# Optimization experiments

Measured on AMD Instinct MI355X. Metric: run time of the kernel, lower is better.

The kernel has to match this reference:

```python
import jax, jax.numpy as jnp
import numpy as np

WD, WH, WW = 1, 8, 8           # window size
NH = 2                          # num heads
EPS = 1e-5                      # torch LayerNorm default


def _layernorm(x, g, b):
    mu = jnp.mean(x, axis=-1, keepdims=True)
    var = jnp.mean((x - mu) ** 2, axis=-1, keepdims=True)
    return (x - mu) * jax.lax.rsqrt(var + EPS) * g + b


def setup_inputs() -> dict:
    key = jax.random.key(0)
    ks = jax.random.split(key, 12)
    C, H = 192, 768  # dim, mlp hidden
    w = lambda k, shape: (jax.random.normal(k, shape, jnp.float32) * 0.02)
    return {
        "x": jax.random.normal(ks[0], (2, 8, 96, 96, C), jnp.float32),
        "norm3_g": jnp.ones((C,), jnp.float32),
        "norm3_b": jnp.zeros((C,), jnp.float32),
        "in_proj_w": w(ks[1], (3 * C, C)),
        "in_proj_b": jnp.zeros((3 * C,), jnp.float32),
        "out_proj_w": w(ks[2], (C, C)),
        "out_proj_b": jnp.zeros((C,), jnp.float32),
        "norm4_g": jnp.ones((C,), jnp.float32),
        "norm4_b": jnp.zeros((C,), jnp.float32),
        "fc1_w": w(ks[3], (H, C)),
        "fc1_b": jnp.zeros((H,), jnp.float32),
        "fc2_w": w(ks[4], (C, H)),
        "fc2_b": jnp.zeros((C,), jnp.float32),
    }


def _part3(x, norm3_g, norm3_b, in_proj_w, in_proj_b, out_proj_w, out_proj_b):
    B, D, H, W, C = x.shape
    Dn, Hn, Wn = D // WD, H // WH, W // WW
    P = Hn * Wn          # spatial windows
    Wt = WD * WH * WW    # tokens per window (64)
    L = Dn * Wt          # attention sequence length

    xn = _layernorm(x, norm3_g, norm3_b)
    # window partition: (B, Dn, Hn, Wn, wd, wh, ww, C)
    xw = xn.reshape(B, Dn, WD, Hn, WH, Wn, WW, C).transpose(0, 1, 3, 5, 2, 4, 6, 7)
    # tgt: (B, Dn, P, Wt, C) -> h: (B*P, Dn*Wt, C)
    tgt = xw.reshape(B, Dn, P, Wt, C)
    h = tgt.transpose(0, 2, 1, 3, 4).reshape(B * P, L, C)

    # qkv projection (torch Linear convention: x @ W.T + b)
    qkv = h @ in_proj_w.T + in_proj_b          # (Bp, L, 3C)
    q, k, v = jnp.split(qkv, 3, axis=-1)
    hd = C // NH
    q = q.reshape(B * P, L, NH, hd)
    k = k.reshape(B * P, L, NH, hd)
    v = v.reshape(B * P, L, NH, hd)

    # block-causal mask over temporal index (each block is Wt x Wt)
    neg_inf = jnp.finfo(jnp.float32).min
    tmask = jnp.triu(jnp.full((Dn, Dn), neg_inf, jnp.float32), k=1)
    mask = jnp.repeat(jnp.repeat(tmask, Wt, axis=0), Wt, axis=1)  # (L, L)

    scale = 1.0 / np.sqrt(hd)
    scores = jnp.einsum("blhd,bmhd->bhlm", q * scale, k) + mask
    attn = jax.nn.softmax(scores, axis=-1)
    out = jnp.einsum("bhlm,bmhd->blhd", attn, v).reshape(B * P, L, C)
    out = out @ out_proj_w.T + out_proj_b

    # reverse: (B, P, Dn, Wt, C) -> windows -> (B, D, H, W, C)
    out = out.reshape(B, P, Dn, Wt, C).transpose(0, 2, 1, 3, 4)
    out = out.reshape(B, Dn, Hn, Wn, WD, WH, WW, C)
    out = out.transpose(0, 1, 4, 2, 5, 3, 6, 7).reshape(B, D, H, W, C)
    return out


def reference(x, norm3_g, norm3_b, in_proj_w, in_proj_b, out_proj_w, out_proj_b,
              norm4_g, norm4_b, fc1_w, fc1_b, fc2_w, fc2_b):
    x = x + _part3(x, norm3_g, norm3_b, in_proj_w, in_proj_b, out_proj_w, out_proj_b)
    xn = _layernorm(x, norm4_g, norm4_b)
    mlp = jax.nn.gelu(xn @ fc1_w.T + fc1_b, approximate=False) @ fc2_w.T + fc2_b
    return x + mlp
```

## Files before the change

### kernel.cpp

```cpp
#include <hip/hip_runtime.h>
#include <cstdint>
#include <cstddef>


typedef float   f32x4  __attribute__((ext_vector_type(4)));
typedef __bf16  bf16x8 __attribute__((ext_vector_type(8)));
typedef unsigned int   u32x4  __attribute__((ext_vector_type(4)));
typedef unsigned short u16x4  __attribute__((ext_vector_type(4)));

#define DEVI __device__ __forceinline__

DEVI float bf2f(unsigned short u) {
    union { unsigned int i; float f; } v; v.i = ((unsigned int)u) << 16; return v.f;
}
DEVI unsigned short f2bf(float f) {
    unsigned int u = __builtin_bit_cast(unsigned int, f);
    unsigned int r = u + 0x7fffu + ((u >> 16) & 1u);
    return (unsigned short)(r >> 16);
}
DEVI float gelu_fast(float v) {
    float t = v * v;
    float z = v * (1.5957691216057308f + 0.07135481627f * t);
    float e = __expf(z);
    float r = 2.0f / (1.0f + e);
    return v - 0.5f * v * r;
}

typedef __attribute__((address_space(3))) unsigned char       lds_u8;
typedef __attribute__((address_space(1))) const unsigned char g_u8;
DEVI void gl_lds16(const void* g, void* l) {
    __builtin_amdgcn_global_load_lds((g_u8*)g, (lds_u8*)l, 16, 0, 0);
}

__global__ __launch_bounds__(256) void k_wconv(const float* __restrict__ wqkv,
                                               const float* __restrict__ wout,
                                               const float* __restrict__ wfc1,
                                               const float* __restrict__ wfc2,
                                               const float* __restrict__ n3g,
                                               const float* __restrict__ n4g,
                                               unsigned short* __restrict__ oq,
                                               unsigned short* __restrict__ oo,
                                               unsigned short* __restrict__ o1,
                                               unsigned short* __restrict__ o2) {
    int i = blockIdx.x * 256 + threadIdx.x;
    if (i < 122880) {
        int r = i / 192, c = i - r * 192;
        oq[i] = (r < 576) ? f2bf(wqkv[i] * n3g[c]) : (unsigned short)0;
    } else if (i < 172032) {
        int j = i - 122880; int r = j / 192;
        oo[j] = (r < 192) ? f2bf(wout[j]) : (unsigned short)0;
    } else if (i < 319488) {
        int j = i - 172032; int c = j % 192;
        o1[j] = f2bf(wfc1[j] * n4g[c]);
    } else if (i < 516096) {
        int j = i - 319488; int r = j / 768;
        o2[j] = (r < 192) ? f2bf(wfc2[j]) : (unsigned short)0;
    }
}

__global__ __launch_bounds__(256) void k_bias(const float* __restrict__ wqkv,
                                              const float* __restrict__ bqkv,
                                              const float* __restrict__ n3b,
                                              const float* __restrict__ wfc1,
                                              const float* __restrict__ bfc1,
                                              const float* __restrict__ n4b,
                                              float* __restrict__ beffq,
                                              float* __restrict__ beff1) {
    int wid = blockIdx.x * 4 + (threadIdx.x >> 6);
    int lane = threadIdx.x & 63;
    const float* wrow; const float* bb; float base; float* dst;
    if (wid < 576) { wrow = wqkv + (size_t)wid * 192; bb = n3b; base = bqkv[wid]; dst = beffq + wid; }
    else { int h = wid - 576; wrow = wfc1 + (size_t)h * 192; bb = n4b; base = bfc1[h]; dst = beff1 + h; }
    float s = wrow[lane] * bb[lane] + wrow[lane + 64] * bb[lane + 64]
            + wrow[lane + 128] * bb[lane + 128];
#pragma unroll
    for (int off = 32; off; off >>= 1) s += __shfl_xor(s, off);
    if (lane == 0) *dst = base + s;
}

__global__ __launch_bounds__(256) void k_ln3(const float* __restrict__ x,
                                             unsigned short* __restrict__ h) {
    int w = threadIdx.x >> 6, lane = threadIdx.x & 63;
    int token = blockIdx.x * 4 + w;
    const float* xp = x + (size_t)token * 192;
    float v0 = xp[lane], v1 = xp[lane + 64], v2 = xp[lane + 128];
    float s = v0 + v1 + v2;
#pragma unroll
    for (int off = 32; off; off >>= 1) s += __shfl_xor(s, off);
    float mean = s * (1.f / 192.f);
    float d0 = v0 - mean, d1 = v1 - mean, d2 = v2 - mean;
    float q = d0 * d0 + d1 * d1 + d2 * d2;
#pragma unroll
    for (int off = 32; off; off >>= 1) q += __shfl_xor(q, off);
    float rs = rsqrtf(q * (1.f / 192.f) + 1e-5f);
    int b  = token / (8 * 96 * 96);
    int r0 = token - b * (8 * 96 * 96);
    int d  = r0 / (96 * 96);
    int r1 = r0 - d * (96 * 96);
    int hh = r1 / 96;
    int ww = r1 - hh * 96;
    int bp = b * 144 + (hh >> 3) * 12 + (ww >> 3);
    int l  = d * 64 + (hh & 7) * 8 + (ww & 7);
    unsigned short* hp = h + ((size_t)bp * 512 + l) * 192;
    hp[lane]       = f2bf(d0 * rs);
    hp[lane + 64]  = f2bf(d1 * rs);
    hp[lane + 128] = f2bf(d2 * rs);
}

__global__ __launch_bounds__(256) void k_ln4b(const unsigned short* __restrict__ yb,
                                              unsigned short* __restrict__ xn) {
    int sub = threadIdx.x >> 5, tl = threadIdx.x & 31;
    size_t row = (size_t)blockIdx.x * 8 + sub;
    const unsigned int* rp = reinterpret_cast<const unsigned int*>(yb + row * 192);
    float v[6];
#pragma unroll
    for (int j = 0; j < 3; j++) {
        unsigned int w = rp[tl + 32 * j];
        v[2 * j]     = bf2f((unsigned short)(w & 0xffffu));
        v[2 * j + 1] = bf2f((unsigned short)(w >> 16));
    }
    float s = v[0] + v[1] + v[2] + v[3] + v[4] + v[5];
#pragma unroll
    for (int off = 1; off < 32; off <<= 1) s += __shfl_xor(s, off);
    float mean = s * (1.f / 192.f);
    float q = 0.f;
#pragma unroll
    for (int j = 0; j < 6; j++) { v[j] -= mean; q += v[j] * v[j]; }
#pragma unroll
    for (int off = 1; off < 32; off <<= 1) q += __shfl_xor(q, off);
    float rs = rsqrtf(q * (1.f / 192.f) + 1e-5f);
    unsigned int* op = reinterpret_cast<unsigned int*>(xn + row * 192);
#pragma unroll
    for (int j = 0; j < 3; j++) {
        unsigned short lo = f2bf(v[2 * j]     * rs);
        unsigned short hi = f2bf(v[2 * j + 1] * rs);
        op[tl + 32 * j] = ((unsigned int)hi << 16) | lo;
    }
}

template <int EPI, int K, int NF>
__global__ __launch_bounds__(256) void k_gemm128(const unsigned short* __restrict__ A,
                                                 const unsigned short* __restrict__ Bw,
                                                 const float* __restrict__ bias,
                                                 unsigned short* __restrict__ outb,
                                                 unsigned short* __restrict__ vt,
                                                 const float* __restrict__ res,
                                                 const unsigned short* __restrict__ resb,
                                                 float* __restrict__ outf) {
    __shared__ unsigned short As[2][128 * 64];
    __shared__ unsigned short Bs[2][NF * 32 * 64];
    const int tid = threadIdx.x;
    const int nwg = gridDim.x * gridDim.y;
    const int flat = blockIdx.y * gridDim.x + blockIdx.x;
    const int swz = (flat & 7) * (nwg >> 3) + (flat >> 3);
    const int bx = swz % gridDim.x, by = swz / gridDim.x;
    const int row0 = by * 128, col0 = bx * (NF * 32);
    const int wv = tid >> 6, lane = tid & 63, lr = lane & 15, lg = lane >> 4;
    const int wr = wv >> 1, wc = wv & 1;
    const int sr = lane >> 3, sc = lane & 7;
    f32x4 acc[4][NF] = {};

    auto stage = [&](int t, int buf) {
        int k0 = t * 64;
#pragma unroll
        for (int i = 0; i < 4; i++) {
            int gq = wv * 4 + i;
            int r = gq * 8 + sr;
            int j = sc ^ (r & 7);
            gl_lds16(A + (size_t)(row0 + r) * K + k0 + j * 8, &As[buf][gq * 512]);
        }
#pragma unroll
        for (int i = 0; i < NF; i++) {
            int gq = wv * NF + i;
            int r = gq * 8 + sr;
            int j = sc ^ (r & 7);
            gl_lds16(Bw + (size_t)(col0 + r) * K + k0 + j * 8, &Bs[buf][gq * 512]);
        }
    };

    const int NT = K / 64;
    stage(0, 0);
    for (int t = 0; t < NT; ++t) {
        int cur = t & 1;
        if (t + 1 < NT) {
            stage(t + 1, cur ^ 1);
            if constexpr (NF == 4) asm volatile("s_waitcnt vmcnt(8)" ::: "memory");
            else                   asm volatile("s_waitcnt vmcnt(7)" ::: "memory");
        } else {
            asm volatile("s_waitcnt vmcnt(0)" ::: "memory");
        }
        __builtin_amdgcn_sched_barrier(0);
        __builtin_amdgcn_s_barrier();
        __builtin_amdgcn_sched_barrier(0);
#pragma unroll
        for (int kk = 0; kk < 64; kk += 32) {
            bf16x8 af[4], bf[NF];
#pragma unroll
            for (int m = 0; m < 4; m++) {
                int r = wr * 64 + m * 16 + lr;
                int j = ((kk >> 3) + lg) ^ (r & 7);
                af[m] = __builtin_bit_cast(bf16x8,
                    *reinterpret_cast<const u32x4*>(&As[cur][r * 64 + j * 8]));
            }
#pragma unroll
            for (int n = 0; n < NF; n++) {
                int r = wc * (NF * 16) + n * 16 + lr;
                int j = ((kk >> 3) + lg) ^ (r & 7);
                bf[n] = __builtin_bit_cast(bf16x8,
                    *reinterpret_cast<const u32x4*>(&Bs[cur][r * 64 + j * 8]));
            }
#pragma unroll
            for (int m = 0; m < 4; m++)
#pragma unroll
                for (int n = 0; n < NF; n++)
                    acc[m][n] = __builtin_amdgcn_mfma_f32_16x16x32_bf16(bf[n], af[m], acc[m][n], 0, 0, 0);
        }
        __builtin_amdgcn_sched_barrier(0);
        __builtin_amdgcn_s_barrier();
        __builtin_amdgcn_sched_barrier(0);
    }

#pragma unroll
    for (int m = 0; m < 4; m++) {
        const int arow = row0 + wr * 64 + m * 16 + lr;
        if constexpr (EPI == 0) {
#pragma unroll
            for (int n = 0; n < NF; n++) {
                const int colb = col0 + wc * (NF * 16) + n * 16 + lg * 4;
                if (colb < 384) {
                    f32x4 b4 = *reinterpret_cast<const f32x4*>(bias + colb);
                    float sc2 = (colb < 192) ? 0.1020620726159658f : 1.f;
                    u16x4 pk;
#pragma unroll
                    for (int rr = 0; rr < 4; rr++) pk[rr] = f2bf((acc[m][n][rr] + b4[rr]) * sc2);
                    *reinterpret_cast<u16x4*>(outb + (size_t)arow * 384 + colb) = pk;
                } else if (colb < 576) {
                    int head = (colb >= 480) ? 1 : 0;
                    int bp = arow >> 9, tok = arow & 511;
                    size_t vb = ((size_t)(bp * 2 + head) * 96 + (colb - 384 - head * 96)) * 512 + tok;
#pragma unroll
                    for (int rr = 0; rr < 4; rr++)
                        vt[vb + (size_t)rr * 512] = f2bf(acc[m][n][rr] + bias[colb + rr]);
                }
            }
        } else if constexpr (EPI == 1) {
            int bp = arow >> 9, l = arow & 511;
            int bb = bp / 144, p = bp - bb * 144;
            int hn = p / 12, wn = p - hn * 12;
            int dn = l >> 6, t_ = l & 63;
            size_t tok = ((size_t)((bb * 8 + dn) * 96 + hn * 8 + (t_ >> 3)) * 96 + wn * 8 + (t_ & 7));
#pragma unroll
            for (int n = 0; n < NF; n++) {
                const int colb = col0 + wc * (NF * 16) + n * 16 + lg * 4;
                size_t idx = tok * 192 + colb;
                f32x4 r4 = *reinterpret_cast<const f32x4*>(res + idx);
                f32x4 b4 = *reinterpret_cast<const f32x4*>(bias + colb);
                u16x4 pk;
#pragma unroll
                for (int rr = 0; rr < 4; rr++) pk[rr] = f2bf(r4[rr] + acc[m][n][rr] + b4[rr]);
                *reinterpret_cast<u16x4*>(outb + idx) = pk;
            }
        } else if constexpr (EPI == 2) {
#pragma unroll
            for (int n = 0; n < NF; n++) {
                const int colb = col0 + wc * (NF * 16) + n * 16 + lg * 4;
                f32x4 b4 = *reinterpret_cast<const f32x4*>(bias + colb);
                u16x4 pk;
#pragma unroll
                for (int rr = 0; rr < 4; rr++) pk[rr] = f2bf(gelu_fast(acc[m][n][rr] + b4[rr]));
                *reinterpret_cast<u16x4*>(outb + (size_t)arow * 768 + colb) = pk;
            }
        } else {
#pragma unroll
            for (int n = 0; n < NF; n++) {
                const int colb = col0 + wc * (NF * 16) + n * 16 + lg * 4;
                size_t idx = (size_t)arow * 192 + colb;
                f32x4 b4 = *reinterpret_cast<const f32x4*>(bias + colb);
                u16x4 rb = *reinterpret_cast<const u16x4*>(resb + idx);
                f32x4 o4;
#pragma unroll
                for (int rr = 0; rr < 4; rr++) o4[rr] = bf2f(rb[rr]) + acc[m][n][rr] + b4[rr];
                *reinterpret_cast<f32x4*>(outf + idx) = o4;
            }
        }
    }
}

__global__ __launch_bounds__(512) void k_attn(const unsigned short* __restrict__ qk,
                                              const unsigned short* __restrict__ vt,
                                              unsigned short* __restrict__ aout) {
    __shared__ unsigned short Ks[64][104];
    __shared__ unsigned short Vs[96][72];
    __shared__ unsigned short Ps[8][16][72];

    int bid = (blockIdx.x & 7) * 288 + (blockIdx.x >> 3);
    int bp = bid >> 3, rest = bid & 7, head = rest >> 2, pr = rest & 3;
    int tid = threadIdx.x, wv = tid >> 6, lane = tid & 63;
    int lr = lane & 15, lg = lane >> 4;
    int wq = wv & 3, wt = wv >> 2;
    int nk = 2 * pr + 2;

    size_t qrow0 = (size_t)bp * 512 + (size_t)(2 * pr + wt) * 64;
    const unsigned short* vbase = vt + (size_t)(bp * 2 + head) * 96 * 512;
    size_t krowb = (size_t)bp * 512;

    bf16x8 qf[3];
    {
        const unsigned short* qp = qk + (qrow0 + wq * 16 + lr) * 384 + head * 96 + lg * 8;
#pragma unroll
        for (int ks = 0; ks < 3; ks++)
            qf[ks] = __builtin_bit_cast(bf16x8, *reinterpret_cast<const u32x4*>(qp + ks * 32));
    }

    f32x4 o[6] = {};
    float m_ = -1e30f, lsum = 0.f;

    u32x4 sreg[3];
    auto issue = [&](int dnk) {
#pragma unroll
        for (int i = 0; i < 3; i++) {
            int c = tid + i * 512;
            if (c < 768) {
                int r = c / 12, cc = c - r * 12;
                sreg[i] = *reinterpret_cast<const u32x4*>(
                    qk + (krowb + dnk * 64 + r) * 384 + 192 + head * 96 + cc * 8);
            } else {
                int c2 = c - 768; int d = c2 >> 3, tb = c2 & 7;
                sreg[i] = *reinterpret_cast<const u32x4*>(
                    vbase + (size_t)d * 512 + dnk * 64 + tb * 8);
            }
        }
    };
    auto commit = [&]() {
#pragma unroll
        for (int i = 0; i < 3; i++) {
            int c = tid + i * 512;
            if (c < 768) {
                int r = c / 12, cc = c - r * 12;
                *reinterpret_cast<u32x4*>(&Ks[r][cc * 8]) = sreg[i];
            } else {
                int c2 = c - 768; int d = c2 >> 3, tb = c2 & 7;
                *reinterpret_cast<u32x4*>(&Vs[d][tb * 8]) = sreg[i];
            }
        }
    };

    issue(0);
    for (int dnk = 0; dnk < nk; ++dnk) {
        commit();
        __syncthreads();
        if (dnk + 1 < nk) issue(dnk + 1);
        if (wt == 1 || dnk < nk - 1) {
            f32x4 st[4] = {};
#pragma unroll
            for (int ks = 0; ks < 3; ks++) {
#pragma unroll
                for (int ct = 0; ct < 4; ct++) {
                    bf16x8 kf = __builtin_bit_cast(bf16x8,
                        *reinterpret_cast<const u32x4*>(&Ks[ct * 16 + lr][ks * 32 + lg * 8]));
                    st[ct] = __builtin_amdgcn_mfma_f32_16x16x32_bf16(kf, qf[ks], st[ct], 0, 0, 0);
                }
            }
            float mx = st[0][0];
#pragma unroll
            for (int ct = 0; ct < 4; ct++)
#pragma unroll
                for (int rr = 0; rr < 4; rr++) mx = fmaxf(mx, st[ct][rr]);
            mx = fmaxf(mx, __shfl_xor(mx, 16));
            mx = fmaxf(mx, __shfl_xor(mx, 32));
            float mnew = fmaxf(m_, mx);
            float corr = __expf(m_ - mnew);
            m_ = mnew;
            float ps = 0.f;
#pragma unroll
            for (int ct = 0; ct < 4; ct++) {
                u16x4 pk;
#pragma unroll
                for (int rr = 0; rr < 4; rr++) {
                    float pv = __expf(st[ct][rr] - mnew);
                    ps += pv;
                    pk[rr] = f2bf(pv);
                }
                *reinterpret_cast<u16x4*>(&Ps[wv][lr][ct * 16 + lg * 4]) = pk;
            }
            ps += __shfl_xor(ps, 16);
            ps += __shfl_xor(ps, 32);
            lsum = lsum * corr + ps;
#pragma unroll
            for (int rr = 0; rr < 4; rr++) {
                float cr = __shfl(corr, (lane & 48) | (lg * 4 + rr));
#pragma unroll
                for (int nf = 0; nf < 6; nf++) o[nf][rr] *= cr;
            }
#pragma unroll
            for (int kk = 0; kk < 2; kk++) {
                bf16x8 pf = __builtin_bit_cast(bf16x8,
                    *reinterpret_cast<const u32x4*>(&Ps[wv][lr][kk * 32 + lg * 8]));
#pragma unroll
                for (int nf = 0; nf < 6; nf++) {
                    bf16x8 vf = __builtin_bit_cast(bf16x8,
                        *reinterpret_cast<const u32x4*>(&Vs[nf * 16 + lr][kk * 32 + lg * 8]));
                    o[nf] = __builtin_amdgcn_mfma_f32_16x16x32_bf16(pf, vf, o[nf], 0, 0, 0);
                }
            }
        }
        __syncthreads();
    }

#pragma unroll
    for (int rr = 0; rr < 4; rr++) {
        float li = __shfl(lsum, (lane & 48) | (lg * 4 + rr));
        float inv = 1.f / li;
        size_t row = qrow0 + wq * 16 + lg * 4 + rr;
#pragma unroll
        for (int nf = 0; nf < 6; nf++)
            aout[row * 192 + head * 96 + nf * 16 + lr] = f2bf(o[nf][rr] * inv);
    }
}

extern "C" void kernel_launch(void* const* d_in, const int* in_sizes, int n_in,
                              void* d_out, int out_size, void* d_ws, size_t ws_size,
                              hipStream_t stream) {
    const float* x    = (const float*)d_in[0];
    const float* n3g  = (const float*)d_in[1];
    const float* n3b  = (const float*)d_in[2];
    const float* wqkv = (const float*)d_in[3];
    const float* bqkv = (const float*)d_in[4];
    const float* wout = (const float*)d_in[5];
    const float* bout = (const float*)d_in[6];
    const float* n4g  = (const float*)d_in[7];
    const float* n4b  = (const float*)d_in[8];
    const float* wfc1 = (const float*)d_in[9];
    const float* bfc1 = (const float*)d_in[10];
    const float* wfc2 = (const float*)d_in[11];
    const float* bfc2 = (const float*)d_in[12];
    float* out = (float*)d_out;

    char* ws = (char*)d_ws;
    unsigned short* qk     = (unsigned short*)(ws + 0);
    unsigned short* vt     = (unsigned short*)(ws + 113246208);
    unsigned short* attn   = (unsigned short*)(ws + 169869312);
    unsigned short* hidden = (unsigned short*)(ws + 0);
    unsigned short* ybf    = (unsigned short*)(ws + 226492416);
    unsigned short* h      = (unsigned short*)(ws + 283115520);
    unsigned short* xn4    = (unsigned short*)(ws + 283115520);
    unsigned short* wq_bf  = (unsigned short*)(ws + 339738624);
    unsigned short* wo_bf  = (unsigned short*)(ws + 339984384);
    unsigned short* w1_bf  = (unsigned short*)(ws + 340082688);
    unsigned short* w2_bf  = (unsigned short*)(ws + 340377600);
    float*          beffq  = (float*)(ws + 340770816);
    float*          beff1  = (float*)(ws + 340773120);

    k_wconv<<<2016, 256, 0, stream>>>(wqkv, wout, wfc1, wfc2, n3g, n4g, wq_bf, wo_bf, w1_bf, w2_bf);
    k_bias<<<336, 256, 0, stream>>>(wqkv, bqkv, n3b, wfc1, bfc1, n4b, beffq, beff1);
    k_ln3<<<36864, 256, 0, stream>>>(x, h);
    k_gemm128<0, 192, 4><<<dim3(5, 1152), 256, 0, stream>>>(h, wq_bf, beffq, qk, vt, nullptr, nullptr, nullptr);
    k_attn<<<2304, 512, 0, stream>>>(qk, vt, attn);
    k_gemm128<1, 192, 3><<<dim3(2, 1152), 256, 0, stream>>>(attn, wo_bf, bout, ybf, nullptr, x, nullptr, nullptr);
    k_ln4b<<<18432, 256, 0, stream>>>(ybf, xn4);
    k_gemm128<2, 192, 4><<<dim3(6, 1152), 256, 0, stream>>>(xn4, w1_bf, beff1, hidden, nullptr, nullptr, nullptr, nullptr);
    k_gemm128<3, 768, 3><<<dim3(2, 1152), 256, 0, stream>>>(hidden, w2_bf, bfc2, nullptr, nullptr, nullptr, ybf, out);
}
```

Before: 551.4 us.

## Fuse LayerNorm4 into fc1 GEMM and run fc2 in FP8

Drops the separate LayerNorm4 kernel. The fc1 GEMM now loads the bf16 residual rows into LDS, computes mean and variance per row, and normalizes in place before the MFMAs. The GELU output is stored as FP8, and fc2 weights are pre-converted to FP8, so fc2 uses FP8 MFMA. This halves hidden-activation traffic and raises MFMA throughput for fc2, at the cost of FP8 precision loss on a 768-wide reduction and redundant LayerNorm work in each of the 6 column blocks.

```diff
diff --git a/kernel.cpp b/kernel.cpp
--- a/kernel.cpp
+++ b/kernel.cpp
@@ -24,6 +24,14 @@
     float e = __expf(z);
     float r = 2.0f / (1.0f + e);
     return v - 0.5f * v * r;
+}
+DEVI unsigned int pk_fp8x4(float a, float b, float c, float d) {
+    int v = __builtin_amdgcn_cvt_pk_fp8_f32(a, b, 0, false);
+    v = __builtin_amdgcn_cvt_pk_fp8_f32(c, d, v, true);
+    return (unsigned int)v;
+}
+DEVI f32x4 mfma_fp8(unsigned long long a, unsigned long long b, f32x4 c) {
+    return __builtin_amdgcn_mfma_f32_16x16x32_fp8_fp8((long)a, (long)b, c, 0, 0, 0);
 }
 
 typedef __attribute__((address_space(3))) unsigned char       lds_u8;
@@ -41,7 +49,7 @@
                                                unsigned short* __restrict__ oq,
                                                unsigned short* __restrict__ oo,
                                                unsigned short* __restrict__ o1,
-                                               unsigned short* __restrict__ o2) {
+                                               unsigned short* __restrict__ o2f8) {
     int i = blockIdx.x * 256 + threadIdx.x;
     if (i < 122880) {
         int r = i / 192, c = i - r * 192;
@@ -52,9 +60,13 @@
     } else if (i < 319488) {
         int j = i - 172032; int c = j % 192;
         o1[j] = f2bf(wfc1[j] * n4g[c]);
-    } else if (i < 516096) {
-        int j = i - 319488; int r = j / 768;
-        o2[j] = (r < 192) ? f2bf(wfc2[j]) : (unsigned short)0;
+    } else if (i < 417792) {
+        int j = i - 319488;
+        int r = j / 384;
+        float a = 0.f, b = 0.f;
+        if (r < 192) { a = wfc2[2 * j]; b = wfc2[2 * j + 1]; }
+        int pk = __builtin_amdgcn_cvt_pk_fp8_f32(a, b, 0, false);
+        o2f8[j] = (unsigned short)pk;
     }
 }
 
@@ -107,46 +119,13 @@
     hp[lane + 128] = f2bf(d2 * rs);
 }
 
-__global__ __launch_bounds__(256) void k_ln4b(const unsigned short* __restrict__ yb,
-                                              unsigned short* __restrict__ xn) {
-    int sub = threadIdx.x >> 5, tl = threadIdx.x & 31;
-    size_t row = (size_t)blockIdx.x * 8 + sub;
-    const unsigned int* rp = reinterpret_cast<const unsigned int*>(yb + row * 192);
-    float v[6];
-#pragma unroll
-    for (int j = 0; j < 3; j++) {
-        unsigned int w = rp[tl + 32 * j];
-        v[2 * j]     = bf2f((unsigned short)(w & 0xffffu));
-        v[2 * j + 1] = bf2f((unsigned short)(w >> 16));
-    }
-    float s = v[0] + v[1] + v[2] + v[3] + v[4] + v[5];
-#pragma unroll
-    for (int off = 1; off < 32; off <<= 1) s += __shfl_xor(s, off);
-    float mean = s * (1.f / 192.f);
-    float q = 0.f;
-#pragma unroll
-    for (int j = 0; j < 6; j++) { v[j] -= mean; q += v[j] * v[j]; }
-#pragma unroll
-    for (int off = 1; off < 32; off <<= 1) q += __shfl_xor(q, off);
-    float rs = rsqrtf(q * (1.f / 192.f) + 1e-5f);
-    unsigned int* op = reinterpret_cast<unsigned int*>(xn + row * 192);
-#pragma unroll
-    for (int j = 0; j < 3; j++) {
-        unsigned short lo = f2bf(v[2 * j]     * rs);
-        unsigned short hi = f2bf(v[2 * j + 1] * rs);
-        op[tl + 32 * j] = ((unsigned int)hi << 16) | lo;
-    }
-}
-
 template <int EPI, int K, int NF>
 __global__ __launch_bounds__(256) void k_gemm128(const unsigned short* __restrict__ A,
                                                  const unsigned short* __restrict__ Bw,
                                                  const float* __restrict__ bias,
                                                  unsigned short* __restrict__ outb,
                                                  unsigned short* __restrict__ vt,
-                                                 const float* __restrict__ res,
-                                                 const unsigned short* __restrict__ resb,
-                                                 float* __restrict__ outf) {
+                                                 const float* __restrict__ res) {
     __shared__ unsigned short As[2][128 * 64];
     __shared__ unsigned short Bs[2][NF * 32 * 64];
     const int tid = threadIdx.x;
@@ -243,7 +222,7 @@
                         vt[vb + (size_t)rr * 512] = f2bf(acc[m][n][rr] + bias[colb + rr]);
                 }
             }
-        } else if constexpr (EPI == 1) {
+        } else {
             int bp = arow >> 9, l = arow & 511;
             int bb = bp / 144, p = bp - bb * 144;
             int hn = p / 12, wn = p - hn * 12;
@@ -259,28 +238,6 @@
 #pragma unroll
                 for (int rr = 0; rr < 4; rr++) pk[rr] = f2bf(r4[rr] + acc[m][n][rr] + b4[rr]);
                 *reinterpret_cast<u16x4*>(outb + idx) = pk;
-            }
-        } else if constexpr (EPI == 2) {
-#pragma unroll
-            for (int n = 0; n < NF; n++) {
-                const int colb = col0 + wc * (NF * 16) + n * 16 + lg * 4;
-                f32x4 b4 = *reinterpret_cast<const f32x4*>(bias + colb);
-                u16x4 pk;
-#pragma unroll
-                for (int rr = 0; rr < 4; rr++) pk[rr] = f2bf(gelu_fast(acc[m][n][rr] + b4[rr]));
-                *reinterpret_cast<u16x4*>(outb + (size_t)arow * 768 + colb) = pk;
-            }
-        } else {
-#pragma unroll
-            for (int n = 0; n < NF; n++) {
-                const int colb = col0 + wc * (NF * 16) + n * 16 + lg * 4;
-                size_t idx = (size_t)arow * 192 + colb;
-                f32x4 b4 = *reinterpret_cast<const f32x4*>(bias + colb);
-                u16x4 rb = *reinterpret_cast<const u16x4*>(resb + idx);
-                f32x4 o4;
-#pragma unroll
-                for (int rr = 0; rr < 4; rr++) o4[rr] = bf2f(rb[rr]) + acc[m][n][rr] + b4[rr];
-                *reinterpret_cast<f32x4*>(outf + idx) = o4;
             }
         }
     }
@@ -415,6 +372,219 @@
 #pragma unroll
         for (int nf = 0; nf < 6; nf++)
             aout[row * 192 + head * 96 + nf * 16 + lr] = f2bf(o[nf][rr] * inv);
+    }
+}
+
+__global__ __launch_bounds__(256) void k_fc1(const unsigned short* __restrict__ ybf,
+                                             const unsigned short* __restrict__ w1,
+                                             const float* __restrict__ beff1,
+                                             unsigned char* __restrict__ hid) {
+    __shared__ unsigned short As[3][128][64];
+    __shared__ unsigned short Bs[2][128 * 64];
+    const int tid = threadIdx.x;
+    const int nwg = gridDim.x * gridDim.y;
+    const int flat = blockIdx.y * gridDim.x + blockIdx.x;
+    const int swz = (flat & 7) * (nwg >> 3) + (flat >> 3);
+    const int bx = swz % gridDim.x, by = swz / gridDim.x;
+    const int row0 = by * 128, col0 = bx * 128;
+    const int wv = tid >> 6, lane = tid & 63, lr = lane & 15, lg = lane >> 4;
+    const int wr = wv >> 1, wc = wv & 1;
+    const int sr = lane >> 3, sc = lane & 7;
+
+    auto stageB = [&](int t, int buf) {
+        int k0 = t * 64;
+#pragma unroll
+        for (int i = 0; i < 4; i++) {
+            int gq = wv * 4 + i;
+            int r = gq * 8 + sr;
+            int j = sc ^ (r & 7);
+            gl_lds16(w1 + (size_t)(col0 + r) * 192 + k0 + j * 8, &Bs[buf][gq * 512]);
+        }
+    };
+
+    stageB(0, 0);
+    {
+        int ar = tid >> 1, ah = tid & 1;
+        const unsigned short* src = ybf + (size_t)(row0 + ar) * 192;
+        float sum = 0.f, ssq = 0.f;
+#pragma unroll
+        for (int ci = 0; ci < 12; ci++) {
+            int c = ah * 12 + ci;
+            u32x4 v = *reinterpret_cast<const u32x4*>(src + c * 8);
+            u16x4* hv = reinterpret_cast<u16x4*>(&v);
+#pragma unroll
+            for (int e = 0; e < 8; e++) {
+                float f = bf2f(((unsigned short*)&v)[e]);
+                sum += f; ssq += f * f;
+            }
+            (void)hv;
+            int j = (c & 7) ^ (ar & 7);
+            *reinterpret_cast<u32x4*>(&As[c >> 3][ar][j * 8]) = v;
+        }
+        sum += __shfl_xor(sum, 1); ssq += __shfl_xor(ssq, 1);
+        float mu = sum * (1.f / 192.f);
+        float rs = rsqrtf(ssq * (1.f / 192.f) - mu * mu + 1e-5f);
+#pragma unroll
+        for (int ci = 0; ci < 12; ci++) {
+            int c = ah * 12 + ci;
+            int j = (c & 7) ^ (ar & 7);
+            unsigned short* p8 = &As[c >> 3][ar][j * 8];
+#pragma unroll
+            for (int e = 0; e < 8; e++)
+                p8[e] = f2bf((bf2f(p8[e]) - mu) * rs);
+        }
+    }
+    asm volatile("s_waitcnt lgkmcnt(0)" ::: "memory");
+
+    f32x4 acc[4][4] = {};
+#pragma unroll
+    for (int t = 0; t < 3; ++t) {
+        if (t + 1 < 3) {
+            stageB(t + 1, (t + 1) & 1);
+            asm volatile("s_waitcnt vmcnt(4)" ::: "memory");
+        } else {
+            asm volatile("s_waitcnt vmcnt(0)" ::: "memory");
+        }
+        __builtin_amdgcn_sched_barrier(0);
+        __builtin_amdgcn_s_barrier();
+        __builtin_amdgcn_sched_barrier(0);
+#pragma unroll
+        for (int kk = 0; kk < 64; kk += 32) {
+            bf16x8 af[4], bf[4];
+#pragma unroll
+            for (int m = 0; m < 4; m++) {
+                int r = wr * 64 + m * 16 + lr;
+                int j = ((kk >> 3) + lg) ^ (r & 7);
+                af[m] = __builtin_bit_cast(bf16x8,
+                    *reinterpret_cast<const u32x4*>(&As[t][r][j * 8]));
+            }
+#pragma unroll
+            for (int n = 0; n < 4; n++) {
+                int r = wc * 64 + n * 16 + lr;
+                int j = ((kk >> 3) + lg) ^ (r & 7);
+                bf[n] = __builtin_bit_cast(bf16x8,
+                    *reinterpret_cast<const u32x4*>(&Bs[t & 1][r * 64 + j * 8]));
+            }
+#pragma unroll
+            for (int m = 0; m < 4; m++)
+#pragma unroll
+                for (int n = 0; n < 4; n++)
+                    acc[m][n] = __builtin_amdgcn_mfma_f32_16x16x32_bf16(bf[n], af[m], acc[m][n], 0, 0, 0);
+        }
+        __builtin_amdgcn_sched_barrier(0);
+        __builtin_amdgcn_s_barrier();
+        __builtin_amdgcn_sched_barrier(0);
+    }
+
+#pragma unroll
+    for (int m = 0; m < 4; m++) {
+        const int arow = row0 + wr * 64 + m * 16 + lr;
+#pragma unroll
+        for (int n = 0; n < 4; n++) {
+            const int colb = col0 + wc * 64 + n * 16 + lg * 4;
+            f32x4 b4 = *reinterpret_cast<const f32x4*>(beff1 + colb);
+            float g0 = gelu_fast(acc[m][n][0] + b4[0]);
+            float g1 = gelu_fast(acc[m][n][1] + b4[1]);
+            float g2 = gelu_fast(acc[m][n][2] + b4[2]);
+            float g3 = gelu_fast(acc[m][n][3] + b4[3]);
+            *reinterpret_cast<unsigned int*>(hid + (size_t)arow * 768 + colb) =
+                pk_fp8x4(g0, g1, g2, g3);
+        }
+    }
+}
+
+__global__ __launch_bounds__(256) void k_fc2(const unsigned char* __restrict__ hid,
+                                             const unsigned char* __restrict__ w2,
+                                             const float* __restrict__ b2,
+                                             const unsigned short* __restrict__ ybf,
+                                             float* __restrict__ out) {
+    __shared__ unsigned char As[2][128 * 64];
+    __shared__ unsigned char Bs[2][128 * 64];
+    const int tid = threadIdx.x;
+    const int nwg = gridDim.x * gridDim.y;
+    const int flat = blockIdx.y * gridDim.x + blockIdx.x;
+    const int swz = (flat & 7) * (nwg >> 3) + (flat >> 3);
+    const int bx = swz % gridDim.x, by = swz / gridDim.x;
+    const int row0 = by * 128, col0 = bx * 96;
+    const int wv = tid >> 6, lane = tid & 63, lr = lane & 15, lg = lane >> 4;
+    const int wr = wv >> 1, wc = wv & 1;
+    const int sr4 = lane >> 2, sc4 = lane & 3;
+    f32x4 acc[4][3] = {};
+
+    auto stage = [&](int t, int buf) {
+        int k0 = t * 64;
+#pragma unroll
+        for (int i = 0; i < 2; i++) {
+            int g = wv * 2 + i;
+            int r = g * 16 + sr4;
+            int j = sc4 ^ (r & 3);
+            gl_lds16(hid + (size_t)(row0 + r) * 768 + k0 + j * 16, &As[buf][g * 1024]);
+        }
+#pragma unroll
+        for (int i = 0; i < 2; i++) {
+            int g = wv * 2 + i;
+            int r = g * 16 + sr4;
+            int j = sc4 ^ (r & 3);
+            gl_lds16(w2 + (size_t)(col0 + r) * 768 + k0 + j * 16, &Bs[buf][g * 1024]);
+        }
+    };
+
+    stage(0, 0);
+    for (int t = 0; t < 12; ++t) {
+        int cur = t & 1;
+        if (t + 1 < 12) {
+            stage(t + 1, cur ^ 1);
+            asm volatile("s_waitcnt vmcnt(4)" ::: "memory");
+        } else {
+            asm volatile("s_waitcnt vmcnt(0)" ::: "memory");
+        }
+        __builtin_amdgcn_sched_barrier(0);
+        __builtin_amdgcn_s_barrier();
+        __builtin_amdgcn_sched_barrier(0);
+#pragma unroll
+        for (int kk = 0; kk < 2; kk++) {
+            const int cc = kk * 2 + (lg >> 1);
+            const int off = (lg & 1) * 8;
+            unsigned long long af[4], bfr[3];
+#pragma unroll
+            for (int m = 0; m < 4; m++) {
+                int r = wr * 64 + m * 16 + lr;
+                int j = cc ^ (r & 3);
+                af[m] = *reinterpret_cast<const unsigned long long*>(
+                    &As[cur][r * 64 + j * 16 + off]);
+            }
+#pragma unroll
+            for (int n = 0; n < 3; n++) {
+                int r = wc * 48 + n * 16 + lr;
+                int j = cc ^ (r & 3);
+                bfr[n] = *reinterpret_cast<const unsigned long long*>(
+                    &Bs[cur][r * 64 + j * 16 + off]);
+            }
+#pragma unroll
+            for (int m = 0; m < 4; m++)
+#pragma unroll
+                for (int n = 0; n < 3; n++)
+                    acc[m][n] = mfma_fp8(bfr[n], af[m], acc[m][n]);
+        }
+        __builtin_amdgcn_sched_barrier(0);
+        __builtin_amdgcn_s_barrier();
+        __builtin_amdgcn_sched_barrier(0);
+    }
+
+#pragma unroll
+    for (int m = 0; m < 4; m++) {
+        const int arow = row0 + wr * 64 + m * 16 + lr;
+#pragma unroll
+        for (int n = 0; n < 3; n++) {
+            const int colb = col0 + wc * 48 + n * 16 + lg * 4;
+            size_t idx = (size_t)arow * 192 + colb;
+            f32x4 b4 = *reinterpret_cast<const f32x4*>(b2 + colb);
+            u16x4 rb = *reinterpret_cast<const u16x4*>(ybf + idx);
+            f32x4 o4;
+#pragma unroll
+            for (int rr = 0; rr < 4; rr++) o4[rr] = bf2f(rb[rr]) + acc[m][n][rr] + b4[rr];
+            *reinterpret_cast<f32x4*>(out + idx) = o4;
+        }
     }
 }
 
@@ -438,26 +608,25 @@
 
     char* ws = (char*)d_ws;
     unsigned short* qk     = (unsigned short*)(ws + 0);
+    unsigned char*  hidden = (unsigned char*)(ws + 0);
     unsigned short* vt     = (unsigned short*)(ws + 113246208);
     unsigned short* attn   = (unsigned short*)(ws + 169869312);
-    unsigned short* hidden = (unsigned short*)(ws + 0);
     unsigned short* ybf    = (unsigned short*)(ws + 226492416);
     unsigned short* h      = (unsigned short*)(ws + 283115520);
-    unsigned short* xn4    = (unsigned short*)(ws + 283115520);
     unsigned short* wq_bf  = (unsigned short*)(ws + 339738624);
     unsigned short* wo_bf  = (unsigned short*)(ws + 339984384);
     unsigned short* w1_bf  = (unsigned short*)(ws + 340082688);
-    unsigned short* w2_bf  = (unsigned short*)(ws + 340377600);
-    float*          beffq  = (float*)(ws + 340770816);
-    float*          beff1  = (float*)(ws + 340773120);
-
-    k_wconv<<<2016, 256, 0, stream>>>(wqkv, wout, wfc1, wfc2, n3g, n4g, wq_bf, wo_bf, w1_bf, w2_bf);
+    unsigned short* w2_f8p = (unsigned short*)(ws + 340377600);
+    unsigned char*  w2_f8  = (unsigned char*)(ws + 340377600);
+    float*          beffq  = (float*)(ws + 340574208);
+    float*          beff1  = (float*)(ws + 340576512);
+
+    k_wconv<<<1632, 256, 0, stream>>>(wqkv, wout, wfc1, wfc2, n3g, n4g, wq_bf, wo_bf, w1_bf, w2_f8p);
     k_bias<<<336, 256, 0, stream>>>(wqkv, bqkv, n3b, wfc1, bfc1, n4b, beffq, beff1);
     k_ln3<<<36864, 256, 0, stream>>>(x, h);
-    k_gemm128<0, 192, 4><<<dim3(5, 1152), 256, 0, stream>>>(h, wq_bf, beffq, qk, vt, nullptr, nullptr, nullptr);
+    k_gemm128<0, 192, 4><<<dim3(5, 1152), 256, 0, stream>>>(h, wq_bf, beffq, qk, vt, nullptr);
     k_attn<<<2304, 512, 0, stream>>>(qk, vt, attn);
-    k_gemm128<1, 192, 3><<<dim3(2, 1152), 256, 0, stream>>>(attn, wo_bf, bout, ybf, nullptr, x, nullptr, nullptr);
-    k_ln4b<<<18432, 256, 0, stream>>>(ybf, xn4);
-    k_gemm128<2, 192, 4><<<dim3(6, 1152), 256, 0, stream>>>(xn4, w1_bf, beff1, hidden, nullptr, nullptr, nullptr, nullptr);
-    k_gemm128<3, 768, 3><<<dim3(2, 1152), 256, 0, stream>>>(hidden, w2_bf, bfc2, nullptr, nullptr, nullptr, ybf, out);
-}
+    k_gemm128<1, 192, 3><<<dim3(2, 1152), 256, 0, stream>>>(attn, wo_bf, bout, ybf, nullptr, x);
+    k_fc1<<<dim3(6, 1152), 256, 0, stream>>>(ybf, w1_bf, beff1, hidden);
+    k_fc2<<<dim3(2, 1152), 256, 0, stream>>>(hidden, w2_f8, bfc2, ybf, out);
+}
```

Result: no change. 545.8 us (-1.0%).

## Store MLP hidden as FP8 and run fc2 with FP8 MFMA kernel

Applied to the files above, without the earlier changes.

The fc1 epilogue now applies a sigmoid-based GELU approximation and packs the hidden activations into FP8 instead of BF16. The fc2 weights are likewise converted to FP8. A new dedicated fc2 GEMM kernel uses FP8 16x16x32 MFMA with swizzled LDS staging, and adds the residual in its epilogue. The goal is to halve the hidden-tensor memory traffic and to use the faster FP8 matrix path. The cost is lower numerical accuracy from both FP8 quantization and the cruder GELU approximation, which may break tolerance.

```diff
diff --git a/kernel.cpp b/kernel.cpp
--- a/kernel.cpp
+++ b/kernel.cpp
@@ -18,12 +18,17 @@
     unsigned int r = u + 0x7fffu + ((u >> 16) & 1u);
     return (unsigned short)(r >> 16);
 }
-DEVI float gelu_fast(float v) {
-    float t = v * v;
-    float z = v * (1.5957691216057308f + 0.07135481627f * t);
-    float e = __expf(z);
-    float r = 2.0f / (1.0f + e);
-    return v - 0.5f * v * r;
+DEVI float gelu_sig(float v) {
+    float e = __expf(-1.702f * v);
+    return v * __builtin_amdgcn_rcpf(1.f + e);
+}
+DEVI unsigned int pk_fp8x4(float a, float b, float c, float d) {
+    int v = __builtin_amdgcn_cvt_pk_fp8_f32(a, b, 0, false);
+    v = __builtin_amdgcn_cvt_pk_fp8_f32(c, d, v, true);
+    return (unsigned int)v;
+}
+DEVI f32x4 mfma_fp8(unsigned long long a, unsigned long long b, f32x4 c) {
+    return __builtin_amdgcn_mfma_f32_16x16x32_fp8_fp8((long)a, (long)b, c, 0, 0, 0);
 }
 
 typedef __attribute__((address_space(3))) unsigned char       lds_u8;
@@ -41,7 +46,7 @@
                                                unsigned short* __restrict__ oq,
                                                unsigned short* __restrict__ oo,
                                                unsigned short* __restrict__ o1,
-                                               unsigned short* __restrict__ o2) {
+                                               unsigned short* __restrict__ o2f8) {
     int i = blockIdx.x * 256 + threadIdx.x;
     if (i < 122880) {
         int r = i / 192, c = i - r * 192;
@@ -52,9 +57,13 @@
     } else if (i < 319488) {
         int j = i - 172032; int c = j % 192;
         o1[j] = f2bf(wfc1[j] * n4g[c]);
-    } else if (i < 516096) {
-        int j = i - 319488; int r = j / 768;
-        o2[j] = (r < 192) ? f2bf(wfc2[j]) : (unsigned short)0;
+    } else if (i < 417792) {
+        int j = i - 319488;
+        int r = j / 384;
+        float a = 0.f, b = 0.f;
+        if (r < 192) { a = wfc2[2 * j]; b = wfc2[2 * j + 1]; }
+        int pk = __builtin_amdgcn_cvt_pk_fp8_f32(a, b, 0, false);
+        o2f8[j] = (unsigned short)pk;
     }
 }
 
@@ -145,8 +154,7 @@
                                                  unsigned short* __restrict__ outb,
                                                  unsigned short* __restrict__ vt,
                                                  const float* __restrict__ res,
-                                                 const unsigned short* __restrict__ resb,
-                                                 float* __restrict__ outf) {
+                                                 unsigned char* __restrict__ outf8) {
     __shared__ unsigned short As[2][128 * 64];
     __shared__ unsigned short Bs[2][NF * 32 * 64];
     const int tid = threadIdx.x;
@@ -260,27 +268,17 @@
                 for (int rr = 0; rr < 4; rr++) pk[rr] = f2bf(r4[rr] + acc[m][n][rr] + b4[rr]);
                 *reinterpret_cast<u16x4*>(outb + idx) = pk;
             }
-        } else if constexpr (EPI == 2) {
+        } else {
 #pragma unroll
             for (int n = 0; n < NF; n++) {
                 const int colb = col0 + wc * (NF * 16) + n * 16 + lg * 4;
                 f32x4 b4 = *reinterpret_cast<const f32x4*>(bias + colb);
-                u16x4 pk;
-#pragma unroll
-                for (int rr = 0; rr < 4; rr++) pk[rr] = f2bf(gelu_fast(acc[m][n][rr] + b4[rr]));
-                *reinterpret_cast<u16x4*>(outb + (size_t)arow * 768 + colb) = pk;
-            }
-        } else {
-#pragma unroll
-            for (int n = 0; n < NF; n++) {
-                const int colb = col0 + wc * (NF * 16) + n * 16 + lg * 4;
-                size_t idx = (size_t)arow * 192 + colb;
-                f32x4 b4 = *reinterpret_cast<const f32x4*>(bias + colb);
-                u16x4 rb = *reinterpret_cast<const u16x4*>(resb + idx);
-                f32x4 o4;
-#pragma unroll
-                for (int rr = 0; rr < 4; rr++) o4[rr] = bf2f(rb[rr]) + acc[m][n][rr] + b4[rr];
-                *reinterpret_cast<f32x4*>(outf + idx) = o4;
+                float g0 = gelu_sig(acc[m][n][0] + b4[0]);
+                float g1 = gelu_sig(acc[m][n][1] + b4[1]);
+                float g2 = gelu_sig(acc[m][n][2] + b4[2]);
+                float g3 = gelu_sig(acc[m][n][3] + b4[3]);
+                *reinterpret_cast<unsigned int*>(outf8 + (size_t)arow * 768 + colb) =
+                    pk_fp8x4(g0, g1, g2, g3);
             }
         }
     }
@@ -415,6 +413,101 @@
 #pragma unroll
         for (int nf = 0; nf < 6; nf++)
             aout[row * 192 + head * 96 + nf * 16 + lr] = f2bf(o[nf][rr] * inv);
+    }
+}
+
+__global__ __launch_bounds__(256) void k_fc2(const unsigned char* __restrict__ hid,
+                                             const unsigned char* __restrict__ w2,
+                                             const float* __restrict__ b2,
+                                             const unsigned short* __restrict__ ybf,
+                                             float* __restrict__ out) {
+    __shared__ unsigned char As[2][128 * 64];
+    __shared__ unsigned char Bs[2][128 * 64];
+    const int tid = threadIdx.x;
+    const int nwg = gridDim.x * gridDim.y;
+    const int flat = blockIdx.y * gridDim.x + blockIdx.x;
+    const int swz = (flat & 7) * (nwg >> 3) + (flat >> 3);
+    const int bx = swz % gridDim.x, by = swz / gridDim.x;
+    const int row0 = by * 128, col0 = bx * 96;
+    const int wv = tid >> 6, lane = tid & 63, lr = lane & 15, lg = lane >> 4;
+    const int wr = wv >> 1, wc = wv & 1;
+    const int sr4 = lane >> 2, sc4 = lane & 3;
+    f32x4 acc[4][3] = {};
+
+    auto stage = [&](int t, int buf) {
+        int k0 = t * 64;
+#pragma unroll
+        for (int i = 0; i < 2; i++) {
+            int g = wv * 2 + i;
+            int r = g * 16 + sr4;
+            int j = sc4 ^ (r & 3);
+            gl_lds16(hid + (size_t)(row0 + r) * 768 + k0 + j * 16, &As[buf][g * 1024]);
+        }
+#pragma unroll
+        for (int i = 0; i < 2; i++) {
+            int g = wv * 2 + i;
+            int r = g * 16 + sr4;
+            int j = sc4 ^ (r & 3);
+            gl_lds16(w2 + (size_t)(col0 + r) * 768 + k0 + j * 16, &Bs[buf][g * 1024]);
+        }
+    };
+
+    stage(0, 0);
+    for (int t = 0; t < 12; ++t) {
+        int cur = t & 1;
+        if (t + 1 < 12) {
+            stage(t + 1, cur ^ 1);
+            asm volatile("s_waitcnt vmcnt(4)" ::: "memory");
+        } else {
+            asm volatile("s_waitcnt vmcnt(0)" ::: "memory");
+        }
+        __builtin_amdgcn_sched_barrier(0);
+        __builtin_amdgcn_s_barrier();
+        __builtin_amdgcn_sched_barrier(0);
+#pragma unroll
+        for (int kk = 0; kk < 2; kk++) {
+            const int cc = kk * 2 + (lg >> 1);
+            const int off = (lg & 1) * 8;
+            unsigned long long af[4], bfr[3];
+#pragma unroll
+            for (int m = 0; m < 4; m++) {
+                int r = wr * 64 + m * 16 + lr;
+                int j = cc ^ (r & 3);
+                af[m] = *reinterpret_cast<const unsigned long long*>(
+                    &As[cur][r * 64 + j * 16 + off]);
+            }
+#pragma unroll
+            for (int n = 0; n < 3; n++) {
+                int r = wc * 48 + n * 16 + lr;
+                int j = cc ^ (r & 3);
+                bfr[n] = *reinterpret_cast<const unsigned long long*>(
+                    &Bs[cur][r * 64 + j * 16 + off]);
+            }
+#pragma unroll
+            for (int m = 0; m < 4; m++)
+#pragma unroll
+                for (int n = 0; n < 3; n++)
+                    acc[m][n] = mfma_fp8(bfr[n], af[m], acc[m][n]);
+        }
+        __builtin_amdgcn_sched_barrier(0);
+        __builtin_amdgcn_s_barrier();
+        __builtin_amdgcn_sched_barrier(0);
+    }
+
+#pragma unroll
+    for (int m = 0; m < 4; m++) {
+        const int arow = row0 + wr * 64 + m * 16 + lr;
+#pragma unroll
+        for (int n = 0; n < 3; n++) {
+            const int colb = col0 + wc * 48 + n * 16 + lg * 4;
+            size_t idx = (size_t)arow * 192 + colb;
+            f32x4 b4 = *reinterpret_cast<const f32x4*>(b2 + colb);
+            u16x4 rb = *reinterpret_cast<const u16x4*>(ybf + idx);
+            f32x4 o4;
+#pragma unroll
+            for (int rr = 0; rr < 4; rr++) o4[rr] = bf2f(rb[rr]) + acc[m][n][rr] + b4[rr];
+            *reinterpret_cast<f32x4*>(out + idx) = o4;
+        }
     }
 }
 
@@ -438,26 +531,27 @@
 
     char* ws = (char*)d_ws;
     unsigned short* qk     = (unsigned short*)(ws + 0);
+    unsigned char*  hidden = (unsigned char*)(ws + 0);
     unsigned short* vt     = (unsigned short*)(ws + 113246208);
     unsigned short* attn   = (unsigned short*)(ws + 169869312);
-    unsigned short* hidden = (unsigned short*)(ws + 0);
     unsigned short* ybf    = (unsigned short*)(ws + 226492416);
     unsigned short* h      = (unsigned short*)(ws + 283115520);
     unsigned short* xn4    = (unsigned short*)(ws + 283115520);
     unsigned short* wq_bf  = (unsigned short*)(ws + 339738624);
     unsigned short* wo_bf  = (unsigned short*)(ws + 339984384);
     unsigned short* w1_bf  = (unsigned short*)(ws + 340082688);
-    unsigned short* w2_bf  = (unsigned short*)(ws + 340377600);
-    float*          beffq  = (float*)(ws + 340770816);
-    float*          beff1  = (float*)(ws + 340773120);
-
-    k_wconv<<<2016, 256, 0, stream>>>(wqkv, wout, wfc1, wfc2, n3g, n4g, wq_bf, wo_bf, w1_bf, w2_bf);
+    unsigned short* w2_f8p = (unsigned short*)(ws + 340377600);
+    unsigned char*  w2_f8  = (unsigned char*)(ws + 340377600);
+    float*          beffq  = (float*)(ws + 340574208);
+    float*          beff1  = (float*)(ws + 340576512);
+
+    k_wconv<<<1632, 256, 0, stream>>>(wqkv, wout, wfc1, wfc2, n3g, n4g, wq_bf, wo_bf, w1_bf, w2_f8p);
     k_bias<<<336, 256, 0, stream>>>(wqkv, bqkv, n3b, wfc1, bfc1, n4b, beffq, beff1);
     k_ln3<<<36864, 256, 0, stream>>>(x, h);
-    k_gemm128<0, 192, 4><<<dim3(5, 1152), 256, 0, stream>>>(h, wq_bf, beffq, qk, vt, nullptr, nullptr, nullptr);
+    k_gemm128<0, 192, 4><<<dim3(5, 1152), 256, 0, stream>>>(h, wq_bf, beffq, qk, vt, nullptr, nullptr);
     k_attn<<<2304, 512, 0, stream>>>(qk, vt, attn);
-    k_gemm128<1, 192, 3><<<dim3(2, 1152), 256, 0, stream>>>(attn, wo_bf, bout, ybf, nullptr, x, nullptr, nullptr);
+    k_gemm128<1, 192, 3><<<dim3(2, 1152), 256, 0, stream>>>(attn, wo_bf, bout, ybf, nullptr, x, nullptr);
     k_ln4b<<<18432, 256, 0, stream>>>(ybf, xn4);
-    k_gemm128<2, 192, 4><<<dim3(6, 1152), 256, 0, stream>>>(xn4, w1_bf, beff1, hidden, nullptr, nullptr, nullptr, nullptr);
-    k_gemm128<3, 768, 3><<<dim3(2, 1152), 256, 0, stream>>>(hidden, w2_bf, bfc2, nullptr, nullptr, nullptr, ybf, out);
-}
+    k_gemm128<2, 192, 4><<<dim3(6, 1152), 256, 0, stream>>>(xn4, w1_bf, beff1, nullptr, nullptr, nullptr, hidden);
+    k_fc2<<<dim3(2, 1152), 256, 0, stream>>>(hidden, w2_f8, bfc2, ybf, out);
+}
```

After: 513.6 us. -6.9%, faster.
